# Kernel optimization log

Measured on AMD Instinct MI355X. Metric: run time of the kernel, lower is better.

Reference implementation:

```python
import jax, jax.numpy as jnp
import numpy as np

H = 16            # num_attention_heads
START_RATIO = 0.1
RECENT_RATIO = 0.4
THETA = 10000.0
CHUNK = 256       # hard-coded chunk_size in source
CLIP = 1e4        # nan_to_num posinf/neginf bound


def _rope_cos_sin(T, D, dtype):
    inv_freq = 1.0 / (THETA ** (jnp.arange(0, D, 2, dtype=jnp.float32) / D))
    freqs = jnp.arange(T, dtype=jnp.float32)[:, None] * inv_freq[None, :]  # [T, D/2]
    emb = jnp.concatenate([freqs, freqs], axis=-1)                          # [T, D]
    return jnp.cos(emb).astype(dtype), jnp.sin(emb).astype(dtype)


def _apply_rope(x, cos, sin):
    # x: [B,H,T,D]; cos/sin: [T,D] broadcast over B,H
    d = x.shape[-1] // 2
    rot = jnp.concatenate([-x[..., d:], x[..., :d]], axis=-1)
    return x * cos + rot * sin


def setup_inputs() -> dict:
    key = jax.random.key(0)
    k0, k1, k2, k3, k4 = jax.random.split(key, 5)
    B, T, Dm = 1, 2048, 2048
    scale = 1.0 / np.sqrt(Dm).astype(np.float32)
    return {
        "hidden_states": jax.random.normal(k0, (B, T, Dm), jnp.float32),
        "Wq": jax.random.normal(k1, (Dm, Dm), jnp.float32) * scale,
        "Wk": jax.random.normal(k2, (Dm, Dm), jnp.float32) * scale,
        "Wv": jax.random.normal(k3, (Dm, Dm), jnp.float32) * scale,
        "Wo": jax.random.normal(k4, (Dm, Dm), jnp.float32) * scale,
    }


def reference(hidden_states, Wq, Wk, Wv, Wo):
    B, T, Dm = hidden_states.shape
    D = Dm // H
    hs = jnp.nan_to_num(hidden_states, nan=0.0, posinf=CLIP, neginf=-CLIP)

    def proj(W):  # torch Linear: x @ W.T, then [B,T,H,D] -> [B,H,T,D]
        return (hs @ W.T).reshape(B, T, H, D).transpose(0, 2, 1, 3)

    q, k, v = proj(Wq), proj(Wk), proj(Wv)
    cos, sin = _rope_cos_sin(T, D, hs.dtype)
    q = _apply_rope(q, cos, sin)
    k = _apply_rope(k, cos, sin)

    # start+recent keep mask (past_key_value=None -> k_len == T)
    k_len = T
    sb = max(0, min(int(START_RATIO * k_len), k_len))
    rb = max(0, min(int(RECENT_RATIO * k_len), k_len - sb))
    pos = jnp.arange(k_len)
    keep = (pos < sb) | (pos >= k_len - rb)          # [K]

    MIN = jnp.finfo(hs.dtype).min
    scores = jnp.einsum('bhqd,bhkd->bhqk', q, k) / jnp.sqrt(jnp.asarray(D, hs.dtype))
    scores = jnp.where(keep, scores, MIN)
    probs = jax.nn.softmax(scores, axis=-1)          # [B,H,T,K]

    # CaM merge of evicted V into recent window, driven by the LAST query row.
    evict = k_len - rb                               # static python int
    last = probs[..., -1, :]                         # [B,H,K]
    mean_attn = last[..., evict + 1:].mean(axis=-1) + 1e-6
    p = jnp.clip(last[..., evict] / mean_attn, 0.0, 1.0)
    p = jnp.nan_to_num(p, nan=0.0, posinf=1.0, neginf=0.0)
    u = jax.random.uniform(jax.random.key(42), p.shape, p.dtype)
    bern = (u < p).astype(v.dtype)                   # [B,H]
    v_e = v[..., evict, :] * bern[..., None] / rb    # [B,H,D]
    v_merged = v.at[..., evict + 1:, :].add(v_e[..., None, :])

    # Chunked loop effect: only the last chunk's AV uses merged V.
    last_start = ((T - 1) // CHUNK) * CHUNK
    out_pre = jnp.einsum('bhqk,bhkd->bhqd', probs[:, :, :last_start], v)
    out_last = jnp.einsum('bhqk,bhkd->bhqd', probs[:, :, last_start:], v_merged)
    out = jnp.concatenate([out_pre, out_last], axis=2)   # [B,H,T,D]

    out = out.transpose(0, 2, 1, 3).reshape(B, T, Dm) @ Wo.T
    return jnp.nan_to_num(out, nan=0.0, posinf=CLIP, neginf=-CLIP)
```

## Files before the change

### kernel.cpp

```cpp
#include <hip/hip_runtime.h>
#include <stdint.h>

#define T_SEQ 2048
#define DM    2048
#define NH    16
#define HD    128
#define SB    204
#define EV    1229
#define RB    819
#define NRECF 818.0f
#define LAST_START 1792
#define SCALE 0.08838834764831845f

typedef __attribute__((ext_vector_type(8))) short short8;
typedef __attribute__((ext_vector_type(4))) short short4v;
typedef __attribute__((ext_vector_type(4))) float f32x4;

__device__ __forceinline__ unsigned short f2bf(float f) {
  uint32_t u = __float_as_uint(f);
  u += 0x7fffu + ((u >> 16) & 1u);
  return (unsigned short)(u >> 16);
}
__device__ __forceinline__ float bf2f(unsigned short s) {
  return __uint_as_float(((uint32_t)s) << 16);
}
__device__ __forceinline__ void gload16(const void* g, void* l) {
  __builtin_amdgcn_global_load_lds((const __attribute__((address_space(1))) void*)g,
                                   (__attribute__((address_space(3))) void*)l,
                                   16, 0, 0);
}
__device__ __forceinline__ float n2n(float v) {
  if (isnan(v)) return 0.0f;
  if (isinf(v)) return v > 0.0f ? 10000.0f : -10000.0f;
  return v;
}

__global__ __launch_bounds__(256) void cvt_kernel(
    const float* __restrict__ hs, const float* __restrict__ wq,
    const float* __restrict__ wk, const float* __restrict__ wv,
    const float* __restrict__ wo, unsigned short* __restrict__ hsb,
    unsigned short* __restrict__ wqb, unsigned short* __restrict__ wkb,
    unsigned short* __restrict__ wvb, unsigned short* __restrict__ wob,
    float* __restrict__ cst, float* __restrict__ snt) {
  if (blockIdx.x >= 20480) {
    int idx = (blockIdx.x - 20480) * 256 + threadIdx.x;
    int t = idx >> 6, i = idx & 63;
    float inv = (float)exp(-(double)i * log(10000.0) / 64.0);
    float ang = (float)t * inv;
    cst[idx] = (float)cos((double)ang);
    snt[idx] = (float)sin((double)ang);
    return;
  }
  int gid = blockIdx.x * 256 + threadIdx.x;
  int region = gid >> 20;
  int off4 = (gid & 1048575) * 4;
  const float* src; unsigned short* dst;
  switch (region) {
    case 0: src = hs; dst = hsb; break;
    case 1: src = wq; dst = wqb; break;
    case 2: src = wk; dst = wkb; break;
    case 3: src = wv; dst = wvb; break;
    default: src = wo; dst = wob; break;
  }
  float4 v = *(const float4*)(src + off4);
  if (region == 0) { v.x = n2n(v.x); v.y = n2n(v.y); v.z = n2n(v.z); v.w = n2n(v.w); }
  ushort4 o;
  o.x = f2bf(v.x); o.y = f2bf(v.y); o.z = f2bf(v.z); o.w = f2bf(v.w);
  *(ushort4*)(dst + off4) = o;
}

__device__ __forceinline__ void gemm_mainloop64(
    const unsigned short* __restrict__ A, const unsigned short* __restrict__ B,
    unsigned short* As, unsigned short* Bs, int m0, int n0, int k0, int ksteps,
    int tid, f32x4 (&acc)[4][4]) {
  int w = tid >> 6, lane = tid & 63;
  int wm = w >> 1, wn = w & 1;
  int q4 = lane >> 4, r = lane & 15;
  f32x4 zero = {0.f, 0.f, 0.f, 0.f};
  #pragma unroll
  for (int mi = 0; mi < 4; mi++)
    #pragma unroll
    for (int ni = 0; ni < 4; ni++) acc[mi][ni] = zero;
  int srow = w * 32 + (lane >> 3);
  int swz = ((lane & 7) ^ (lane >> 3)) * 16;
  const char* Ag = (const char*)(A + (size_t)(m0 + srow) * DM) + swz + k0 * 2;
  const char* Bg = (const char*)(B + (size_t)(n0 + srow) * DM) + swz + k0 * 2;
  unsigned short* Asl = As + w * 2048;
  unsigned short* Bsl = Bs + w * 2048;
  for (int s = 0; s < ksteps; s++) {
    __syncthreads();
    #pragma unroll
    for (int g = 0; g < 4; g++) {
      gload16(Ag + g * (8 * DM * 2), Asl + g * 512);
      gload16(Bg + g * (8 * DM * 2), Bsl + g * 512);
    }
    Ag += 128; Bg += 128;
    __syncthreads();
    #pragma unroll
    for (int kh = 0; kh < 2; kh++) {
      int pcs = ((kh * 4 + q4) ^ (r & 7)) * 8;
      short8 a[4], b[4];
      #pragma unroll
      for (int mi = 0; mi < 4; mi++)
        a[mi] = *(const short8*)(As + (wm * 64 + mi * 16 + r) * 64 + pcs);
      #pragma unroll
      for (int ni = 0; ni < 4; ni++)
        b[ni] = *(const short8*)(Bs + ((ni & 1) * 64 + wn * 32 + (ni >> 1) * 16 + r) * 64 + pcs);
      #pragma unroll
      for (int mi = 0; mi < 4; mi++)
        #pragma unroll
        for (int ni = 0; ni < 4; ni++)
          acc[mi][ni] = __builtin_amdgcn_mfma_f32_16x16x32_bf16(a[mi], b[ni], acc[mi][ni], 0, 0, 0);
    }
  }
}

__global__ __launch_bounds__(256, 3) void gemm_qkv_kernel(
    const unsigned short* __restrict__ hsb, const unsigned short* __restrict__ wqb,
    const unsigned short* __restrict__ wkb, const unsigned short* __restrict__ wvb,
    const float* __restrict__ cst, const float* __restrict__ snt,
    unsigned short* __restrict__ qbf, unsigned short* __restrict__ kbf,
    unsigned short* __restrict__ vbT) {
  __shared__ __align__(16) unsigned short LDSBUF[17408];
  unsigned short* As = LDSBUF;
  unsigned short* Bs = LDSBUF + 8192;
  int y = blockIdx.y;
  int z, mi;
  if (y < 16)      { z = 0; mi = y; }
  else if (y < 25) { z = 1; mi = y - 16; }
  else             { z = 2; mi = y - 25; }
  if (z) mi = (mi < 2) ? mi : mi + 7;
  const unsigned short* B = (z == 0) ? wqb : (z == 1) ? wkb : wvb;
  int m0 = mi * 128, n0 = blockIdx.x * 128;
  f32x4 acc[4][4];
  gemm_mainloop64(hsb, B, As, Bs, m0, n0, 0, DM / 64, threadIdx.x, acc);
  int tid = threadIdx.x, w = tid >> 6, lane = tid & 63;
  int wm = w >> 1, wn = w & 1, q4 = lane >> 4, r = lane & 15;
  int h = n0 >> 7;
  if (z < 2) {
    unsigned short* dst = (z == 0) ? qbf : kbf;
    #pragma unroll
    for (int mj = 0; mj < 4; mj++)
      #pragma unroll
      for (int p = 0; p < 2; p++) {
        int d = wn * 32 + p * 16 + r;
        #pragma unroll
        for (int g = 0; g < 4; g++) {
          int t = m0 + wm * 64 + mj * 16 + q4 * 4 + g;
          float c = cst[t * 64 + d], s = snt[t * 64 + d];
          float x0 = acc[mj][2 * p][g], x1 = acc[mj][2 * p + 1][g];
          dst[((size_t)h * T_SEQ + t) * HD + d]      = f2bf(x0 * c - x1 * s);
          dst[((size_t)h * T_SEQ + t) * HD + d + 64] = f2bf(x1 * c + x0 * s);
        }
      }
  } else {
    __syncthreads();
    #pragma unroll
    for (int mj = 0; mj < 4; mj++)
      #pragma unroll
      for (int ni = 0; ni < 4; ni++) {
        int c = (ni & 1) * 64 + wn * 32 + (ni >> 1) * 16 + r;
        int tl = wm * 64 + mj * 16 + q4 * 4;
        short4v pv;
        pv[0] = (short)f2bf(acc[mj][ni][0]);
        pv[1] = (short)f2bf(acc[mj][ni][1]);
        pv[2] = (short)f2bf(acc[mj][ni][2]);
        pv[3] = (short)f2bf(acc[mj][ni][3]);
        *(short4v*)(LDSBUF + c * 136 + tl) = pv;
      }
    __syncthreads();
    int d = tid >> 1, th = tid & 1;
    unsigned short* gdst = vbT + ((size_t)h * HD + d) * T_SEQ + m0 + th * 64;
    const unsigned short* lsrc = LDSBUF + d * 136 + th * 64;
    #pragma unroll
    for (int j = 0; j < 8; j++)
      *(short8*)(gdst + j * 8) = *(const short8*)(lsrc + j * 8);
  }
}

__device__ __forceinline__ void attn_body2(
    int kb, const unsigned short* Kt0, const unsigned short* Kt1,
    const unsigned short* Vt0, const unsigned short* Vt1,
    const unsigned short* ind0, const unsigned short* ind1,
    unsigned short* Ps0, unsigned short* Ps1,
    const short8 (&aq)[4], f32x4 (&o)[8], f32x4& o9, float (&evf)[4],
    int q4, int r) {
  f32x4 zero = {0.f, 0.f, 0.f, 0.f};
  int rsw = (r >> 1) & 3;
  f32x4 sA0 = zero, sA1 = zero, sB0 = zero, sB1 = zero;
  __builtin_amdgcn_s_setprio(1);
  #pragma unroll
  for (int c = 0; c < 4; c++) {
    int pc = ((c * 4 + q4) ^ r) * 8;
    short8 kA0 = *(const short8*)(Kt0 + r * 128 + pc);
    short8 kA1 = *(const short8*)(Kt0 + (16 + r) * 128 + pc);
    short8 kB0 = *(const short8*)(Kt1 + r * 128 + pc);
    short8 kB1 = *(const short8*)(Kt1 + (16 + r) * 128 + pc);
    sA0 = __builtin_amdgcn_mfma_f32_16x16x32_bf16(aq[c], kA0, sA0, 0, 0, 0);
    sA1 = __builtin_amdgcn_mfma_f32_16x16x32_bf16(aq[c], kA1, sA1, 0, 0, 0);
    sB0 = __builtin_amdgcn_mfma_f32_16x16x32_bf16(aq[c], kB0, sB0, 0, 0, 0);
    sB1 = __builtin_amdgcn_mfma_f32_16x16x32_bf16(aq[c], kB1, sB1, 0, 0, 0);
  }
  __builtin_amdgcn_s_setprio(0);
  int kgA0 = kb + r, kgA1 = kb + 16 + r, kgB0 = kb + 32 + r, kgB1 = kb + 48 + r;
  bool keepA0 = (kgA0 < SB) || (kgA0 >= EV);
  bool keepA1 = (kgA1 < SB) || (kgA1 >= EV);
  bool keepB0 = (kgB0 < SB) || (kgB0 >= EV);
  bool keepB1 = (kgB1 < SB) || (kgB1 >= EV);
  #pragma unroll
  for (int g = 0; g < 4; g++) {
    float pA0 = keepA0 ? __expf(fmaf(sA0[g], SCALE, -8.0f)) : 0.0f;
    float pA1 = keepA1 ? __expf(fmaf(sA1[g], SCALE, -8.0f)) : 0.0f;
    float pB0 = keepB0 ? __expf(fmaf(sB0[g], SCALE, -8.0f)) : 0.0f;
    float pB1 = keepB1 ? __expf(fmaf(sB1[g], SCALE, -8.0f)) : 0.0f;
    if (kb == 1216 && kgA0 == EV) evf[g] = pA0;
    int row = q4 * 4 + g;
    int psw = (row >> 1) & 3;
    int c0 = (((r >> 3) ^ psw) * 8) + (r & 7);
    int c1 = ((((r >> 3) + 2) ^ psw) * 8) + (r & 7);
    Ps0[row * 32 + c0] = f2bf(pA0);
    Ps0[row * 32 + c1] = f2bf(pA1);
    Ps1[row * 32 + c0] = f2bf(pB0);
    Ps1[row * 32 + c1] = f2bf(pB1);
  }
  short8 pa0 = *(const short8*)(Ps0 + r * 32 + (q4 ^ rsw) * 8);
  short8 pa1 = *(const short8*)(Ps1 + r * 32 + (q4 ^ rsw) * 8);
  __builtin_amdgcn_s_setprio(1);
  #pragma unroll
  for (int ni = 0; ni < 8; ni++) {
    short8 bv0 = *(const short8*)(Vt0 + (ni * 16 + r) * 32 + (q4 ^ rsw) * 8);
    short8 bv1 = *(const short8*)(Vt1 + (ni * 16 + r) * 32 + (q4 ^ rsw) * 8);
    o[ni] = __builtin_amdgcn_mfma_f32_16x16x32_bf16(pa0, bv0, o[ni], 0, 0, 0);
    o[ni] = __builtin_amdgcn_mfma_f32_16x16x32_bf16(pa1, bv1, o[ni], 0, 0, 0);
  }
  short8 bi0 = *(const short8*)(ind0 + r * 32 + (q4 ^ rsw) * 8);
  short8 bi1 = *(const short8*)(ind1 + r * 32 + (q4 ^ rsw) * 8);
  o9 = __builtin_amdgcn_mfma_f32_16x16x32_bf16(pa0, bi0, o9, 0, 0, 0);
  o9 = __builtin_amdgcn_mfma_f32_16x16x32_bf16(pa1, bi1, o9, 0, 0, 0);
  __builtin_amdgcn_s_setprio(0);
}

__global__ __launch_bounds__(256, 2) void attn_kernel(
    const unsigned short* __restrict__ qbf, const unsigned short* __restrict__ kbf,
    const unsigned short* __restrict__ vbT, unsigned short* __restrict__ atb,
    float* __restrict__ attnf_s, float* __restrict__ Ssum, float* __restrict__ lst) {
  __shared__ __align__(16) unsigned short KtS[2][2][4096];
  __shared__ __align__(16) unsigned short VtS[2][2][4096];
  __shared__ __align__(16) unsigned short Ps[4][2][512];
  __shared__ __align__(16) unsigned short Ind[3 * 512];
  int tid = threadIdx.x, w = tid >> 6, lane = tid & 63;
  int q4 = lane >> 4, r = lane & 15;
  int bid = blockIdx.x;
  int xcd = bid & 7, j = bid >> 3;
  int h = xcd * 2 + (j >> 5);
  int qx = j & 31;
  int qb = qx * 64 + w * 16;

  for (int idx = tid; idx < 3 * 512; idx += 256) {
    int v = idx >> 9, n = (idx >> 5) & 15, jj = idx & 31;
    float val = 0.f;
    if (n == 0) val = 1.f;
    else if (n == 1) val = (v == 1) ? (jj >= 14 ? 1.f : 0.f) : (v == 2 ? 1.f : 0.f);
    Ind[v * 512 + n * 32 + (((jj >> 3) ^ ((n >> 1) & 3)) * 8) + (jj & 7)] = f2bf(val);
  }

  short8 aq[4];
  {
    const unsigned short* qrow = qbf + ((size_t)h * T_SEQ + qb + r) * HD;
    #pragma unroll
    for (int c = 0; c < 4; c++) aq[c] = *(const short8*)(qrow + c * 32 + q4 * 8);
  }
  f32x4 zero = {0.f, 0.f, 0.f, 0.f};
  f32x4 o[8], o9;
  #pragma unroll
  for (int ni = 0; ni < 8; ni++) o[ni] = zero;
  o9 = zero;
  float evf[4] = {0.f, 0.f, 0.f, 0.f};

  const char* Kbase = (const char*)(kbf + (size_t)h * T_SEQ * HD);
  int krow0 = w * 8 + q4, krow1 = krow0 + 4;
  const char* Kg0 = Kbase + krow0 * 256 + ((r ^ (krow0 & 15)) * 16);
  const char* Kg1 = Kbase + krow1 * 256 + ((r ^ (krow1 & 15)) * 16);
  const char* Vbase = (const char*)(vbT + (size_t)h * HD * T_SEQ);
  int vsrc = ((lane & 3) ^ ((lane >> 3) & 3)) * 16;
  const char* Vg0 = Vbase + (size_t)(w * 32 + (lane >> 2)) * 4096 + vsrc;
  const char* Vg1 = Vg0 + 16 * 4096;

  auto issue_chunk = [&](int ci, int db) {
    int kb = (ci < 4) ? ci * 64 : 1216 + (ci - 4) * 64;
    gload16(Kg0 + kb * 256,         &KtS[db][0][w * 1024]);
    gload16(Kg1 + kb * 256,         &KtS[db][0][w * 1024 + 512]);
    gload16(Kg0 + (kb + 32) * 256,  &KtS[db][1][w * 1024]);
    gload16(Kg1 + (kb + 32) * 256,  &KtS[db][1][w * 1024 + 512]);
    gload16(Vg0 + kb * 2,           &VtS[db][0][w * 1024]);
    gload16(Vg1 + kb * 2,           &VtS[db][0][w * 1024 + 512]);
    gload16(Vg0 + (kb + 32) * 2,    &VtS[db][1][w * 1024]);
    gload16(Vg1 + (kb + 32) * 2,    &VtS[db][1][w * 1024 + 512]);
  };

  issue_chunk(0, 0);
  for (int ci = 0; ci < 17; ci++) {
    int db = ci & 1;
    int kb = (ci < 4) ? ci * 64 : 1216 + (ci - 4) * 64;
    const unsigned short* indA = Ind + ((ci < 4) ? 0 : (ci == 4) ? 512 : 1024);
    const unsigned short* indB = Ind + ((ci < 4) ? 0 : 1024);
    __syncthreads();
    if (ci < 16) issue_chunk(ci + 1, db ^ 1);
    attn_body2(kb, KtS[db][0], KtS[db][1], VtS[db][0], VtS[db][1],
               indA, indB, &Ps[w][0][0], &Ps[w][1][0], aq, o, o9, evf, q4, r);
  }

  float invl[4], srn[4], evn[4];
  #pragma unroll
  for (int g = 0; g < 4; g++) {
    float l  = __shfl(o9[g], lane & 48, 64);
    float sr = __shfl(o9[g], (lane & 48) | 1, 64);
    float ev = __shfl(evf[g], (lane & 48) | 13, 64);
    invl[g] = 1.0f / l;
    srn[g] = sr * invl[g];
    evn[g] = ev * invl[g];
  }
  if (qx < (LAST_START / 64)) {
    #pragma unroll
    for (int ni = 0; ni < 8; ni++)
      #pragma unroll
      for (int g = 0; g < 4; g++)
        atb[(size_t)(qb + q4 * 4 + g) * DM + h * HD + ni * 16 + r] = f2bf(o[ni][g] * invl[g]);
  } else {
    #pragma unroll
    for (int ni = 0; ni < 8; ni++)
      #pragma unroll
      for (int g = 0; g < 4; g++)
        attnf_s[(size_t)(qb - LAST_START + q4 * 4 + g) * DM + h * HD + ni * 16 + r] = o[ni][g] * invl[g];
  }
  if (r == 0) {
    #pragma unroll
    for (int g = 0; g < 4; g++) {
      int t = qb + q4 * 4 + g;
      if (t >= LAST_START) Ssum[h * 256 + (t - LAST_START)] = srn[g];
      if (t == T_SEQ - 1) { lst[h * 2] = evn[g]; lst[h * 2 + 1] = srn[g]; }
    }
  }
}

__device__ __forceinline__ void tf_round(uint32_t& x0, uint32_t& x1, int rot) {
  x0 += x1;
  x1 = (x1 << rot) | (x1 >> (32 - rot));
  x1 ^= x0;
}
__device__ __forceinline__ float bern_scale(int hh, const float* lst) {
  const uint32_t k0 = 0u, k1 = 42u, k2 = 0x1BD11BDAu ^ k0 ^ k1;
  uint32_t x0 = (uint32_t)(hh & 7), x1 = (uint32_t)((hh & 7) + 8);
  x0 += k0; x1 += k1;
  tf_round(x0, x1, 13); tf_round(x0, x1, 15); tf_round(x0, x1, 26); tf_round(x0, x1, 6);
  x0 += k1; x1 += k2 + 1u;
  tf_round(x0, x1, 17); tf_round(x0, x1, 29); tf_round(x0, x1, 16); tf_round(x0, x1, 24);
  x0 += k2; x1 += k0 + 2u;
  tf_round(x0, x1, 13); tf_round(x0, x1, 15); tf_round(x0, x1, 26); tf_round(x0, x1, 6);
  x0 += k0; x1 += k1 + 3u;
  tf_round(x0, x1, 17); tf_round(x0, x1, 29); tf_round(x0, x1, 16); tf_round(x0, x1, 24);
  x0 += k1; x1 += k2 + 4u;
  tf_round(x0, x1, 13); tf_round(x0, x1, 15); tf_round(x0, x1, 26); tf_round(x0, x1, 6);
  x0 += k2; x1 += k0 + 5u;
  uint32_t bits = (hh < 8) ? x0 : x1;
  float u = __uint_as_float((bits >> 9) | 0x3f800000u) - 1.0f;
  float evp = lst[hh * 2], srp = lst[hh * 2 + 1];
  float mean = srp * (1.0f / NRECF) + 1e-6f;
  float p = evp / mean;
  p = fminf(fmaxf(p, 0.0f), 1.0f);
  if (!(p == p)) p = 0.0f;
  return (u < p) ? (1.0f / (float)RB) : 0.0f;
}

__global__ __launch_bounds__(256) void fixup_kernel(
    const float* __restrict__ attnf_s, const float* __restrict__ Ssum,
    const float* __restrict__ lst, const unsigned short* __restrict__ vbT,
    unsigned short* __restrict__ atb) {
  int idx = blockIdx.x * 256 + threadIdx.x;
  int t2 = idx >> 11, n = idx & 2047;
  int h = n >> 7, d = n & 127;
  float bsc = bern_scale(h, lst);
  float v = attnf_s[idx];
  v += Ssum[h * 256 + t2] * bsc * bf2f(vbT[((size_t)h * HD + d) * T_SEQ + EV]);
  atb[(size_t)(t2 + LAST_START) * DM + n] = f2bf(v);
}

__global__ __launch_bounds__(512, 2) void gemm_out_kernel(
    const unsigned short* __restrict__ atb, const unsigned short* __restrict__ wob,
    float* __restrict__ out) {
  __shared__ __align__(16) unsigned short LDSBUF[32768];
  int tid = threadIdx.x;
  int grp = tid >> 8;
  int ltid = tid & 255;
  unsigned short* As = LDSBUF + grp * 16384;
  unsigned short* Bs = As + 8192;
  int m0 = blockIdx.y * 128, n0 = blockIdx.x * 128;
  f32x4 acc[4][4];
  gemm_mainloop64(atb, wob, As, Bs, m0, n0, grp * 1024, 16, ltid, acc);
  float* Cx = (float*)LDSBUF;
  __syncthreads();
  if (grp) {
    #pragma unroll
    for (int mi = 0; mi < 4; mi++)
      #pragma unroll
      for (int ni = 0; ni < 4; ni++)
        #pragma unroll
        for (int g = 0; g < 4; g++)
          Cx[(mi * 16 + ni * 4 + g) * 256 + ltid] = acc[mi][ni][g];
  }
  __syncthreads();
  if (!grp) {
    int w = ltid >> 6, lane = ltid & 63;
    int wm = w >> 1, wn = w & 1, q4 = lane >> 4, r = lane & 15;
    #pragma unroll
    for (int mi = 0; mi < 4; mi++)
      #pragma unroll
      for (int ni = 0; ni < 4; ni++) {
        int c = n0 + (ni & 1) * 64 + wn * 32 + (ni >> 1) * 16 + r;
        #pragma unroll
        for (int g = 0; g < 4; g++) {
          int t = m0 + wm * 64 + mi * 16 + q4 * 4 + g;
          out[(size_t)t * DM + c] = n2n(acc[mi][ni][g] + Cx[(mi * 16 + ni * 4 + g) * 256 + ltid]);
        }
      }
  }
}

extern "C" void kernel_launch(void* const* d_in, const int* in_sizes, int n_in,
                              void* d_out, int out_size, void* d_ws, size_t ws_size,
                              hipStream_t stream) {
  const float* hs = (const float*)d_in[0];
  const float* Wq = (const float*)d_in[1];
  const float* Wk = (const float*)d_in[2];
  const float* Wv = (const float*)d_in[3];
  const float* Wo = (const float*)d_in[4];
  char* ws = (char*)d_ws;
  const size_t MB = 1024 * 1024;
  unsigned short* hsb = (unsigned short*)(ws + 0);
  unsigned short* wqb = (unsigned short*)(ws + 8 * MB);
  unsigned short* wkb = (unsigned short*)(ws + 16 * MB);
  unsigned short* wvb = (unsigned short*)(ws + 24 * MB);
  unsigned short* wob = (unsigned short*)(ws + 32 * MB);
  unsigned short* qbf = (unsigned short*)(ws + 40 * MB);
  unsigned short* kbf = (unsigned short*)(ws + 48 * MB);
  unsigned short* vbT = (unsigned short*)(ws + 56 * MB);
  unsigned short* atb = (unsigned short*)(ws + 64 * MB);
  float* attnf_s = (float*)(ws + 72 * MB);
  float* cst = (float*)(ws + 106 * MB);
  float* snt = (float*)(ws + 106 * MB + 524288);
  float* Ssum = (float*)(ws + 107 * MB);
  float* lst = (float*)(ws + 107 * MB + 16384);

  cvt_kernel<<<20992, 256, 0, stream>>>(hs, Wq, Wk, Wv, Wo, hsb, wqb, wkb, wvb, wob, cst, snt);
  gemm_qkv_kernel<<<dim3(16, 34), 256, 0, stream>>>(hsb, wqb, wkb, wvb, cst, snt, qbf, kbf, vbT);
  attn_kernel<<<512, 256, 0, stream>>>(qbf, kbf, vbT, atb, attnf_s, Ssum, lst);
  fixup_kernel<<<2048, 256, 0, stream>>>(attnf_s, Ssum, lst, vbT, atb);
  gemm_out_kernel<<<dim3(16, 16), 512, 0, stream>>>(atb, wob, (float*)d_out);
}
```

Before: 237.9 us.

## Widen attention blocks to 128 queries, vectorize fixup, use float sincos for RoPE

The attention kernel now runs 8 waves per block covering 128 query rows, so each K/V tile loaded into LDS is shared by twice as many queries and global K/V traffic is halved. Each wave issues half as many async loads per chunk, and the grid shrinks to 256 blocks. The fixup kernel processes four elements per thread with float4 loads and ushort4 stores. RoPE table generation switches from double-precision exp, cos and sin to exp2f and sincosf, which may lose slight accuracy at large angles.

Result: no change. 233.4 us (-1.9%).

```diff
diff --git a/kernel.cpp b/kernel.cpp
--- a/kernel.cpp
+++ b/kernel.cpp
@@ -45,10 +45,12 @@
   if (blockIdx.x >= 20480) {
     int idx = (blockIdx.x - 20480) * 256 + threadIdx.x;
     int t = idx >> 6, i = idx & 63;
-    float inv = (float)exp(-(double)i * log(10000.0) / 64.0);
+    float inv = exp2f(-(float)i * 0.20761871929904988f);
     float ang = (float)t * inv;
-    cst[idx] = (float)cos((double)ang);
-    snt[idx] = (float)sin((double)ang);
+    float s, c;
+    sincosf(ang, &s, &c);
+    cst[idx] = c;
+    snt[idx] = s;
     return;
   }
   int gid = blockIdx.x * 256 + threadIdx.x;
@@ -240,23 +242,23 @@
   __builtin_amdgcn_s_setprio(0);
 }
 
-__global__ __launch_bounds__(256, 2) void attn_kernel(
+__global__ __launch_bounds__(512, 1) void attn_kernel(
     const unsigned short* __restrict__ qbf, const unsigned short* __restrict__ kbf,
     const unsigned short* __restrict__ vbT, unsigned short* __restrict__ atb,
     float* __restrict__ attnf_s, float* __restrict__ Ssum, float* __restrict__ lst) {
   __shared__ __align__(16) unsigned short KtS[2][2][4096];
   __shared__ __align__(16) unsigned short VtS[2][2][4096];
-  __shared__ __align__(16) unsigned short Ps[4][2][512];
+  __shared__ __align__(16) unsigned short Ps[8][2][512];
   __shared__ __align__(16) unsigned short Ind[3 * 512];
-  int tid = threadIdx.x, w = tid >> 6, lane = tid & 63;
+  int tid = threadIdx.x, w8 = tid >> 6, lane = tid & 63;
   int q4 = lane >> 4, r = lane & 15;
   int bid = blockIdx.x;
   int xcd = bid & 7, j = bid >> 3;
-  int h = xcd * 2 + (j >> 5);
-  int qx = j & 31;
-  int qb = qx * 64 + w * 16;
-
-  for (int idx = tid; idx < 3 * 512; idx += 256) {
+  int h = xcd * 2 + (j >> 4);
+  int qx = j & 15;
+  int qb = qx * 128 + w8 * 16;
+
+  for (int idx = tid; idx < 3 * 512; idx += 512) {
     int v = idx >> 9, n = (idx >> 5) & 15, jj = idx & 31;
     float val = 0.f;
     if (n == 0) val = 1.f;
@@ -278,24 +280,18 @@
   float evf[4] = {0.f, 0.f, 0.f, 0.f};
 
   const char* Kbase = (const char*)(kbf + (size_t)h * T_SEQ * HD);
-  int krow0 = w * 8 + q4, krow1 = krow0 + 4;
-  const char* Kg0 = Kbase + krow0 * 256 + ((r ^ (krow0 & 15)) * 16);
-  const char* Kg1 = Kbase + krow1 * 256 + ((r ^ (krow1 & 15)) * 16);
+  int krow = w8 * 4 + q4;
+  const char* Kg = Kbase + krow * 256 + ((r ^ (krow & 15)) * 16);
   const char* Vbase = (const char*)(vbT + (size_t)h * HD * T_SEQ);
   int vsrc = ((lane & 3) ^ ((lane >> 3) & 3)) * 16;
-  const char* Vg0 = Vbase + (size_t)(w * 32 + (lane >> 2)) * 4096 + vsrc;
-  const char* Vg1 = Vg0 + 16 * 4096;
+  const char* Vg = Vbase + (size_t)(w8 * 16 + (lane >> 2)) * 4096 + vsrc;
 
   auto issue_chunk = [&](int ci, int db) {
     int kb = (ci < 4) ? ci * 64 : 1216 + (ci - 4) * 64;
-    gload16(Kg0 + kb * 256,         &KtS[db][0][w * 1024]);
-    gload16(Kg1 + kb * 256,         &KtS[db][0][w * 1024 + 512]);
-    gload16(Kg0 + (kb + 32) * 256,  &KtS[db][1][w * 1024]);
-    gload16(Kg1 + (kb + 32) * 256,  &KtS[db][1][w * 1024 + 512]);
-    gload16(Vg0 + kb * 2,           &VtS[db][0][w * 1024]);
-    gload16(Vg1 + kb * 2,           &VtS[db][0][w * 1024 + 512]);
-    gload16(Vg0 + (kb + 32) * 2,    &VtS[db][1][w * 1024]);
-    gload16(Vg1 + (kb + 32) * 2,    &VtS[db][1][w * 1024 + 512]);
+    gload16(Kg + kb * 256,        &KtS[db][0][w8 * 512]);
+    gload16(Kg + (kb + 32) * 256, &KtS[db][1][w8 * 512]);
+    gload16(Vg + kb * 2,          &VtS[db][0][w8 * 512]);
+    gload16(Vg + (kb + 32) * 2,   &VtS[db][1][w8 * 512]);
   };
 
   issue_chunk(0, 0);
@@ -307,7 +303,7 @@
     __syncthreads();
     if (ci < 16) issue_chunk(ci + 1, db ^ 1);
     attn_body2(kb, KtS[db][0], KtS[db][1], VtS[db][0], VtS[db][1],
-               indA, indB, &Ps[w][0][0], &Ps[w][1][0], aq, o, o9, evf, q4, r);
+               indA, indB, &Ps[w8][0][0], &Ps[w8][1][0], aq, o, o9, evf, q4, r);
   }
 
   float invl[4], srn[4], evn[4];
@@ -320,7 +316,7 @@
     srn[g] = sr * invl[g];
     evn[g] = ev * invl[g];
   }
-  if (qx < (LAST_START / 64)) {
+  if (qx < 14) {
     #pragma unroll
     for (int ni = 0; ni < 8; ni++)
       #pragma unroll
@@ -376,13 +372,18 @@
     const float* __restrict__ attnf_s, const float* __restrict__ Ssum,
     const float* __restrict__ lst, const unsigned short* __restrict__ vbT,
     unsigned short* __restrict__ atb) {
-  int idx = blockIdx.x * 256 + threadIdx.x;
+  int idx = (blockIdx.x * 256 + threadIdx.x) * 4;
   int t2 = idx >> 11, n = idx & 2047;
   int h = n >> 7, d = n & 127;
-  float bsc = bern_scale(h, lst);
-  float v = attnf_s[idx];
-  v += Ssum[h * 256 + t2] * bsc * bf2f(vbT[((size_t)h * HD + d) * T_SEQ + EV]);
-  atb[(size_t)(t2 + LAST_START) * DM + n] = f2bf(v);
+  float bsc = bern_scale(h, lst) * Ssum[h * 256 + t2];
+  float4 v = *(const float4*)(attnf_s + idx);
+  const unsigned short* vrow = vbT + ((size_t)h * HD + d) * T_SEQ + EV;
+  ushort4 ov;
+  ov.x = f2bf(v.x + bsc * bf2f(vrow[0]));
+  ov.y = f2bf(v.y + bsc * bf2f(vrow[T_SEQ]));
+  ov.z = f2bf(v.z + bsc * bf2f(vrow[2 * T_SEQ]));
+  ov.w = f2bf(v.w + bsc * bf2f(vrow[3 * T_SEQ]));
+  *(ushort4*)(atb + (size_t)(t2 + LAST_START) * DM + n) = ov;
 }
 
 __global__ __launch_bounds__(512, 2) void gemm_out_kernel(
@@ -453,7 +454,7 @@
 
   cvt_kernel<<<20992, 256, 0, stream>>>(hs, Wq, Wk, Wv, Wo, hsb, wqb, wkb, wvb, wob, cst, snt);
   gemm_qkv_kernel<<<dim3(16, 34), 256, 0, stream>>>(hsb, wqb, wkb, wvb, cst, snt, qbf, kbf, vbT);
-  attn_kernel<<<512, 256, 0, stream>>>(qbf, kbf, vbT, atb, attnf_s, Ssum, lst);
-  fixup_kernel<<<2048, 256, 0, stream>>>(attnf_s, Ssum, lst, vbT, atb);
+  attn_kernel<<<256, 512, 0, stream>>>(qbf, kbf, vbT, atb, attnf_s, Ssum, lst);
+  fixup_kernel<<<512, 256, 0, stream>>>(attnf_s, Ssum, lst, vbT, atb);
   gemm_out_kernel<<<dim3(16, 16), 512, 0, stream>>>(atb, wob, (float*)d_out);
 }
```
